# Kernel tuning notes

Hardware: AMD Instinct MI355X
Metric: run time of the kernel (lower is better)

The kernel has to match this reference:

```python
import jax, jax.numpy as jnp
import numpy as np

K = 5        # kernel_size per pseudo-dim
DIM = 2      # pseudo-coordinate dimensionality
K2 = K * K   # total kernel weight matrices
N_NODES = 50000


def spline_basis(edge_attr):
    """Open B-spline basis, degree=1, dim=2. Returns basis [E,4], weight_index [E,4]."""
    v = edge_attr * (K - 1)                      # [E,2], pseudo in [0,1]
    lo = jnp.floor(v)
    frac = v - lo                                # [E,2]
    lo = lo.astype(jnp.int32)
    fac = jnp.stack([1.0 - frac, frac], axis=-1)                 # [E,2,2] (dim, bit)
    idx = jnp.clip(lo[..., None] + jnp.arange(2), 0, K - 1)      # [E,2,2]
    b0 = jnp.array([0, 1, 0, 1])  # bit for dim 0, per spline term
    b1 = jnp.array([0, 0, 1, 1])  # bit for dim 1
    basis = fac[:, 0, b0] * fac[:, 1, b1]        # [E,4]
    wi = idx[:, 0, b0] * K + idx[:, 1, b1]       # [E,4] flat kernel index
    return basis, wi


def spline_conv(x, src, dst, basis, wi, W, root, bias, n_nodes):
    """SplineConv with mean aggregation, root weight and bias.
    x:[N,Fin] W:[K2,Fin,Fout] root:[Fin,Fout] bias:[Fout]"""
    E = src.shape[0]
    K2_, Fin, Fout = W.shape
    # scatter the 4 sparse basis values into a dense per-edge kernel-coeff matrix [E,K2]
    coeff = jnp.zeros((E, K2_), x.dtype).at[jnp.arange(E)[:, None], wi].add(basis)
    xj = x[src]                                  # gather source features [E,Fin]
    msg = jnp.zeros((E, Fout), x.dtype)
    for k in range(K2_):                         # fixed small loop over 25 kernels
        msg = msg + coeff[:, k:k + 1] * (xj @ W[k])
    agg = jax.ops.segment_sum(msg, dst, num_segments=n_nodes)    # [N,Fout]
    deg = jax.ops.segment_sum(jnp.ones((E,), x.dtype), dst, num_segments=n_nodes)
    agg = agg / jnp.clip(deg, 1.0)[:, None]      # mean aggregation
    return agg + x @ root + bias


def setup_inputs() -> dict:
    key = jax.random.key(0)
    ks = jax.random.split(key, 9)
    E = 800000
    Fin, H, C = 64, 16, 7
    x = jax.random.normal(ks[0], (N_NODES, Fin), dtype=jnp.float32)
    edge_index = jax.random.randint(ks[1], (2, E), 0, N_NODES, dtype=jnp.int64)
    edge_attr = jax.random.uniform(ks[2], (E, DIM), dtype=jnp.float32)
    s1 = 1.0 / np.sqrt(Fin)
    s2 = 1.0 / np.sqrt(H)
    W1 = jax.random.uniform(ks[3], (K2, Fin, H), jnp.float32, -s1, s1)
    root1 = jax.random.uniform(ks[4], (Fin, H), jnp.float32, -s1, s1)
    bias1 = jax.random.uniform(ks[5], (H,), jnp.float32, -s1, s1)
    W2 = jax.random.uniform(ks[6], (K2, H, C), jnp.float32, -s2, s2)
    root2 = jax.random.uniform(ks[7], (H, C), jnp.float32, -s2, s2)
    bias2 = jax.random.uniform(ks[8], (C,), jnp.float32, -s2, s2)
    return {"x": x, "edge_index": edge_index, "edge_attr": edge_attr,
            "W1": W1, "root1": root1, "bias1": bias1,
            "W2": W2, "root2": root2, "bias2": bias2}


def reference(x, edge_index, edge_attr, W1, root1, bias1, W2, root2, bias2):
    src = edge_index[0]
    dst = edge_index[1]
    basis, wi = spline_basis(edge_attr)
    h = jax.nn.relu(spline_conv(x, src, dst, basis, wi, W1, root1, bias1, N_NODES))
    # dropout(p=0.6) is identity in eval mode
    out = spline_conv(h, src, dst, basis, wi, W2, root2, bias2, N_NODES)
    return jax.nn.log_softmax(out, axis=1)
```

## Files before the change

### kernel.cpp

```cpp
#include <hip/hip_runtime.h>

#define KK2 25
#define FIN 64
#define HH 16
#define CC 7

#define SCAN_VPT 4
#define SCAN_BLK 256
#define SCAN_CHUNK (SCAN_VPT * SCAN_BLK)

__device__ inline unsigned short f2bf(float f) {
    unsigned u = __float_as_uint(f);
    return (unsigned short)((u + 0x7FFFu + ((u >> 16) & 1u)) >> 16);
}
__device__ inline float bf2f(unsigned short b) {
    return __uint_as_float(((unsigned)b) << 16);
}

__global__ void k_hist(const int* __restrict__ ei, int* __restrict__ cnt, int E) {
    int e = blockIdx.x * 256 + threadIdx.x;
    if (e < E) atomicAdd(&cnt[ei[E + e]], 1);
}

__global__ void k_bsum(const int* __restrict__ cnt, int* __restrict__ bsum, int N) {
    int b = blockIdx.x, t = threadIdx.x;
    int base = b * SCAN_CHUNK + t * SCAN_VPT;
    int s = 0;
#pragma unroll
    for (int j = 0; j < SCAN_VPT; j++) {
        int i = base + j;
        if (i < N) s += cnt[i];
    }
#pragma unroll
    for (int d = 1; d < 64; d <<= 1) s += __shfl_xor(s, d, 64);
    __shared__ int sd[SCAN_BLK / 64];
    if ((t & 63) == 0) sd[t >> 6] = s;
    __syncthreads();
    if (t == 0) {
        int tot = 0;
        for (int w = 0; w < SCAN_BLK / 64; w++) tot += sd[w];
        bsum[b] = tot;
    }
}

__global__ void k_bscan(const int* __restrict__ bsum, int* __restrict__ boff, int nblk) {
    int t = threadIdx.x;
    __shared__ int sd[256];
    int v = (t < nblk) ? bsum[t] : 0;
    sd[t] = v;
    __syncthreads();
    for (int off = 1; off < 256; off <<= 1) {
        int u = (t >= off) ? sd[t - off] : 0;
        __syncthreads();
        sd[t] += u;
        __syncthreads();
    }
    boff[t] = sd[t] - v;
}

__global__ void k_sfin(const int* __restrict__ cnt, const int* __restrict__ boff,
                       int* __restrict__ rowStart, int* __restrict__ cursor, int N) {
    int b = blockIdx.x, t = threadIdx.x;
    int base = b * SCAN_CHUNK + t * SCAN_VPT;
    int v[SCAN_VPT];
    int s = 0;
#pragma unroll
    for (int j = 0; j < SCAN_VPT; j++) {
        int i = base + j;
        v[j] = (i < N) ? cnt[i] : 0;
        s += v[j];
    }
    __shared__ int sd[SCAN_BLK];
    sd[t] = s;
    __syncthreads();
    for (int off = 1; off < SCAN_BLK; off <<= 1) {
        int u = (t >= off) ? sd[t - off] : 0;
        __syncthreads();
        sd[t] += u;
        __syncthreads();
    }
    int run = sd[t] - s + boff[b];
#pragma unroll
    for (int j = 0; j < SCAN_VPT; j++) {
        int i = base + j;
        if (i < N) {
            rowStart[i] = run;
            cursor[i] = run;
            run += v[j];
            if (i == N - 1) rowStart[N] = run;
        }
    }
}

__global__ void k_scatter(const float* __restrict__ attr, const int* __restrict__ ei,
                          int* __restrict__ cursor, uint4* __restrict__ rec, int E) {
    int e = blockIdx.x * 256 + threadIdx.x;
    if (e >= E) return;
    float v0 = attr[2 * e] * 4.0f, v1 = attr[2 * e + 1] * 4.0f;
    float l0 = floorf(v0), l1 = floorf(v1);
    float f0 = v0 - l0, f1 = v1 - l1;
    int i0 = (int)l0, i1 = (int)l1;
    int i0a = min(max(i0, 0), 4), i0b = min(max(i0 + 1, 0), 4);
    int i1a = min(max(i1, 0), 4);
    float bx = (1.0f - f0) * (1.0f - f1);
    float by = f0 * (1.0f - f1);
    float bz = (1.0f - f0) * f1;
    float bw = f0 * f1;
    unsigned pA = (unsigned)(i0a * 5 + i1a);
    unsigned pB = (unsigned)(i0b * 5 + i1a);
    int s = ei[e], d = ei[E + e];
    int pos = atomicAdd(&cursor[d], 1);
    uint4 r;
    r.x = (unsigned)f2bf(bx) | ((unsigned)f2bf(by) << 16);
    r.y = (unsigned)f2bf(bz) | ((unsigned)f2bf(bw) << 16);
    r.z = (unsigned)s;
    r.w = pA | (pB << 8);
    rec[pos] = r;
}

__global__ void k_prepW(const float* __restrict__ W1, const float* __restrict__ W2,
                        float* __restrict__ B1t, float* __restrict__ W2p) {
    int tid = blockIdx.x * 256 + threadIdx.x;
    if (tid < KK2 * FIN * HH) {
        int c = tid >> 6, i = tid & 63;
        int k = c >> 4, h = c & 15;
        B1t[tid] = W1[(k * FIN + i) * HH + h];
    }
    if (tid < KK2 * HH * 8) {
        int k = tid >> 7, r = tid & 127;
        int i = r >> 3, c = r & 7;
        W2p[tid] = (c < CC) ? W2[(k * HH + i) * CC + c] : 0.0f;
    }
}

__global__ void k_y1(const float* __restrict__ x, const float* __restrict__ B1t,
                     unsigned short* __restrict__ y1q, int N, int nbl) {
    __shared__ uint4 sh[4][2][144];
    int i0 = blockIdx.x / nbl;
    int nwin = blockIdx.x % nbl;
    int n = nwin * 256 + threadIdx.x;
    int wv = threadIdx.x >> 6, lane = threadIdx.x & 63;
    bool active = (n < N);
    float4 xr[16];
    if (active) {
        const float4* xp = (const float4*)(x + (size_t)n * 64);
#pragma unroll
        for (int i = 0; i < 16; i++) xr[i] = xp[i];
    }
    int nwb = nwin * 256 + wv * 64;
    int validf = min(64, max(0, N - nwb)) * 4;
    size_t NN = (size_t)N;

    for (int i1 = 0; i1 < 5; i1++) {
        int k = i0 * 5 + i1;
        const float* B = B1t + k * 16 * 64;
        unsigned tmp[8];
        if (active) {
#pragma unroll
            for (int h4 = 0; h4 < 4; h4++) {
                float a0 = 0, a1 = 0, a2 = 0, a3 = 0;
                const float4* b0 = (const float4*)(B + (h4 * 4 + 0) * 64);
                const float4* b1 = (const float4*)(B + (h4 * 4 + 1) * 64);
                const float4* b2 = (const float4*)(B + (h4 * 4 + 2) * 64);
                const float4* b3 = (const float4*)(B + (h4 * 4 + 3) * 64);
#pragma unroll
                for (int i = 0; i < 16; i++) {
                    float4 xi = xr[i];
                    float4 v0 = b0[i], v1 = b1[i], v2 = b2[i], v3 = b3[i];
                    a0 += xi.x * v0.x + xi.y * v0.y + xi.z * v0.z + xi.w * v0.w;
                    a1 += xi.x * v1.x + xi.y * v1.y + xi.z * v1.z + xi.w * v1.w;
                    a2 += xi.x * v2.x + xi.y * v2.y + xi.z * v2.z + xi.w * v2.w;
                    a3 += xi.x * v3.x + xi.y * v3.y + xi.z * v3.z + xi.w * v3.w;
                }
                tmp[h4 * 2 + 0] = (unsigned)f2bf(a0) | ((unsigned)f2bf(a1) << 16);
                tmp[h4 * 2 + 1] = (unsigned)f2bf(a2) | ((unsigned)f2bf(a3) << 16);
            }
        } else {
#pragma unroll
            for (int j = 0; j < 8; j++) tmp[j] = 0;
        }
        int slot = i1 & 1;
        int i0e = lane * 2, i1e = lane * 2 + 1;
        sh[wv][slot][i0e + (i0e >> 3)] = make_uint4(tmp[0], tmp[1], tmp[2], tmp[3]);
        sh[wv][slot][i1e + (i1e >> 3)] = make_uint4(tmp[4], tmp[5], tmp[6], tmp[7]);
        __syncthreads();
        if (i1 >= 1) {
            int p = i0 * 5 + (i1 - 1);
            uint4* g4 = (uint4*)(y1q + ((size_t)p * NN + nwb) * 32);
#pragma unroll
            for (int j = 0; j < 4; j++) {
                int f = j * 64 + lane;
                if (f < validf) {
                    int node = f >> 2, piece = f & 3;
                    int idx = node * 2 + (piece & 1);
                    int ss = (piece < 2) ? (slot ^ 1) : slot;
                    g4[f] = sh[wv][ss][idx + (idx >> 3)];
                }
            }
        }
        if (i1 == 4) {
            int p = i0 * 5 + 4;
            uint4* g4 = (uint4*)(y1q + ((size_t)p * NN + nwb) * 32);
#pragma unroll
            for (int j = 0; j < 4; j++) {
                int f = j * 64 + lane;
                if (f < validf) {
                    int node = f >> 2, piece = f & 3;
                    int idx = node * 2 + (piece & 1);
                    g4[f] = sh[wv][slot][idx + (idx >> 3)];
                }
            }
        }
        __syncthreads();
    }
}

__global__ void k_agg1u(const int* __restrict__ rowStart, const uint4* __restrict__ rec,
                        const unsigned short* __restrict__ y1q, const float* __restrict__ x,
                        const float* __restrict__ root1, const float* __restrict__ bias1,
                        float* __restrict__ h1, int N) {
    int n = blockIdx.x * 4 + (threadIdx.x >> 6);
    if (n >= N) return;
    int lane = threadIdx.x & 63;
    int sub = lane >> 4, h = lane & 15;
    int start = rowStart[n], end = rowStart[n + 1];
    float acc = 0.0f;
    size_t NN = (size_t)N;
    for (int i = start + sub; i < end; i += 4) {
        uint4 r = rec[i];
        float bx = bf2f((unsigned short)(r.x & 0xffffu));
        float by = bf2f((unsigned short)(r.x >> 16));
        float bz = bf2f((unsigned short)(r.y & 0xffffu));
        float bw = bf2f((unsigned short)(r.y >> 16));
        int s = (int)r.z;
        unsigned w = r.w;
        const unsigned short* rA = y1q + ((w & 255u) * NN + s) * 32;
        const unsigned short* rB = y1q + (((w >> 8) & 255u) * NN + s) * 32;
        acc += bx * bf2f(rA[h]) + bz * bf2f(rA[16 + h]);
        acc += by * bf2f(rB[h]) + bw * bf2f(rB[16 + h]);
    }
    acc += __shfl_xor(acc, 16, 64);
    acc += __shfl_xor(acc, 32, 64);
    float inv = 1.0f / (float)max(end - start, 1);
    float rv = acc * inv + bias1[h];
    const float* xrow = x + (size_t)n * 64;
#pragma unroll 8
    for (int i = 0; i < 64; i++) rv += xrow[i] * root1[i * 16 + h];
    rv = fmaxf(rv, 0.0f);
    if (lane < 16) h1[(size_t)n * 16 + h] = rv;
}

__global__ void k_y2(const float* __restrict__ h1, const float* __restrict__ W2p,
                     unsigned short* __restrict__ y2Tb, int N, int nbl) {
    int kg = blockIdx.x / nbl;
    int n = (blockIdx.x % nbl) * 256 + threadIdx.x;
    if (n >= N) return;
    float hreg[16];
    const float4* hp = (const float4*)(h1 + (size_t)n * 16);
#pragma unroll
    for (int j = 0; j < 4; j++) {
        float4 v = hp[j];
        hreg[4 * j] = v.x; hreg[4 * j + 1] = v.y;
        hreg[4 * j + 2] = v.z; hreg[4 * j + 3] = v.w;
    }
#pragma unroll
    for (int dk = 0; dk < 5; dk++) {
        int k = kg * 5 + dk;
        float z[8] = {0, 0, 0, 0, 0, 0, 0, 0};
        const float4* wp = (const float4*)(W2p + k * 128);
#pragma unroll
        for (int i = 0; i < 16; i++) {
            float hi = hreg[i];
            float4 lo = wp[2 * i], hv = wp[2 * i + 1];
            z[0] += hi * lo.x; z[1] += hi * lo.y; z[2] += hi * lo.z; z[3] += hi * lo.w;
            z[4] += hi * hv.x; z[5] += hi * hv.y; z[6] += hi * hv.z; z[7] += hi * hv.w;
        }
        uint4 p;
        p.x = (unsigned)f2bf(z[0]) | ((unsigned)f2bf(z[1]) << 16);
        p.y = (unsigned)f2bf(z[2]) | ((unsigned)f2bf(z[3]) << 16);
        p.z = (unsigned)f2bf(z[4]) | ((unsigned)f2bf(z[5]) << 16);
        p.w = (unsigned)f2bf(z[6]) | ((unsigned)f2bf(z[7]) << 16);
        *(uint4*)(y2Tb + ((size_t)k * N + n) * 8) = p;
    }
}

__global__ void k_agg2f(const int* __restrict__ rowStart, const uint4* __restrict__ rec,
                        const unsigned short* __restrict__ y2Tb, const float* __restrict__ h1,
                        const float* __restrict__ root2, const float* __restrict__ bias2,
                        float* __restrict__ out, int N) {
    int n = blockIdx.x * 4 + (threadIdx.x >> 6);
    if (n >= N) return;
    int lane = threadIdx.x & 63;
    int sub = lane >> 3, c = lane & 7;
    int start = rowStart[n], end = rowStart[n + 1];
    float acc = 0.0f;
    size_t NN = (size_t)N;
    for (int i = start + sub; i < end; i += 8) {
        uint4 r = rec[i];
        float bx = bf2f((unsigned short)(r.x & 0xffffu));
        float by = bf2f((unsigned short)(r.x >> 16));
        float bz = bf2f((unsigned short)(r.y & 0xffffu));
        float bw = bf2f((unsigned short)(r.y >> 16));
        int s = (int)r.z;
        unsigned pA = r.w & 255u, pB = (r.w >> 8) & 255u;
        unsigned i1a = pA % 5u;
        unsigned d = (i1a < 4u) ? 1u : 0u;
        acc += bx * bf2f(y2Tb[(pA * NN + s) * 8 + c]);
        acc += by * bf2f(y2Tb[(pB * NN + s) * 8 + c]);
        acc += bz * bf2f(y2Tb[((pA + d) * NN + s) * 8 + c]);
        acc += bw * bf2f(y2Tb[((pB + d) * NN + s) * 8 + c]);
    }
    acc += __shfl_xor(acc, 8, 64);
    acc += __shfl_xor(acc, 16, 64);
    acc += __shfl_xor(acc, 32, 64);
    float inv = 1.0f / (float)max(end - start, 1);
    float z;
    if (c < CC) {
        z = acc * inv + bias2[c];
        const float* hrow = h1 + (size_t)n * 16;
#pragma unroll
        for (int i = 0; i < 16; i++) z += hrow[i] * root2[i * CC + c];
    } else {
        z = -1e30f;
    }
    float m = z;
    m = fmaxf(m, __shfl_xor(m, 1, 64));
    m = fmaxf(m, __shfl_xor(m, 2, 64));
    m = fmaxf(m, __shfl_xor(m, 4, 64));
    float ex = (c < CC) ? expf(z - m) : 0.0f;
    float ssum = ex;
    ssum += __shfl_xor(ssum, 1, 64);
    ssum += __shfl_xor(ssum, 2, 64);
    ssum += __shfl_xor(ssum, 4, 64);
    float ls = logf(ssum);
    if (lane < CC) out[(size_t)n * 7 + c] = z - m - ls;
}

extern "C" void kernel_launch(void* const* d_in, const int* in_sizes, int n_in,
                              void* d_out, int out_size, void* d_ws, size_t ws_size,
                              hipStream_t stream) {
    const float* x     = (const float*)d_in[0];
    const int*   ei    = (const int*)d_in[1];
    const float* attr  = (const float*)d_in[2];
    const float* W1    = (const float*)d_in[3];
    const float* root1 = (const float*)d_in[4];
    const float* bias1 = (const float*)d_in[5];
    const float* W2    = (const float*)d_in[6];
    const float* root2 = (const float*)d_in[7];
    const float* bias2 = (const float*)d_in[8];
    float* out = (float*)d_out;

    int N = in_sizes[0] / FIN;
    int E = in_sizes[1] / 2;

    char* w = (char*)d_ws;
    size_t off = 0;
    auto alloc = [&](size_t bytes) -> void* {
        void* p = w + off;
        off += (bytes + 255) & ~(size_t)255;
        return p;
    };
    int*      cnt      = (int*)alloc((size_t)N * 4);
    int*      rowStart = (int*)alloc((size_t)(N + 1) * 4);
    int*      cursor   = (int*)alloc((size_t)N * 4);
    int*      bsum     = (int*)alloc(260 * 4);
    int*      boff     = (int*)alloc(260 * 4);
    uint4*    rec      = (uint4*)alloc((size_t)E * 16);
    float*    h1       = (float*)alloc((size_t)N * 64);
    float*    B1t      = (float*)alloc((size_t)KK2 * FIN * HH * 4);
    float*    W2p      = (float*)alloc((size_t)KK2 * HH * 8 * 4);
    unsigned short* y1q  = (unsigned short*)alloc((size_t)KK2 * N * 32 * 2);
    unsigned short* y2Tb = y1q;
    (void)ws_size; (void)n_in; (void)out_size;

    hipMemsetAsync(cnt, 0, (size_t)N * 4, stream);

    int ebl = (E + 255) / 256;
    int nbl = (N + 255) / 256;
    int sblk = (N + SCAN_CHUNK - 1) / SCAN_CHUNK;

    k_hist<<<ebl, 256, 0, stream>>>(ei, cnt, E);
    k_bsum<<<sblk, SCAN_BLK, 0, stream>>>(cnt, bsum, N);
    k_bscan<<<1, 256, 0, stream>>>(bsum, boff, sblk);
    k_sfin<<<sblk, SCAN_BLK, 0, stream>>>(cnt, boff, rowStart, cursor, N);
    k_scatter<<<ebl, 256, 0, stream>>>(attr, ei, cursor, rec, E);
    k_prepW<<<(KK2 * FIN * HH + 255) / 256, 256, 0, stream>>>(W1, W2, B1t, W2p);
    k_y1<<<5 * nbl, 256, 0, stream>>>(x, B1t, y1q, N, nbl);
    k_agg1u<<<(N + 3) / 4, 256, 0, stream>>>(rowStart, rec, y1q, x, root1, bias1, h1, N);
    k_y2<<<5 * nbl, 256, 0, stream>>>(h1, W2p, y2Tb, N, nbl);
    k_agg2f<<<(N + 3) / 4, 256, 0, stream>>>(rowStart, rec, y2Tb, h1, root2, bias2, out, N);
}
```

Before: 289.2 us.

## Store layer-1 per-kernel projections node-major and unroll edge gather loop

Changes the y1 intermediate from kernel-major [K2][N][32] to node-major [N][800] bf16, so all 25 kernel projections of a source node sit contiguously. The layer-1 gather then reads both kernel rows for an edge from the same 1.6 KB node block, which should improve cache and DRAM locality. The aggregation loop is also unrolled by two edges per lane-group with separate accumulators to raise memory-level parallelism. The k_y1 writes become strided by 100 uint4 per node, so that write pass loses its coalescing. y2Tb still aliases the buffer and k_y2 is unchanged.

```diff
diff --git a/kernel.cpp b/kernel.cpp
--- a/kernel.cpp
+++ b/kernel.cpp
@@ -134,7 +134,7 @@
 }
 
 __global__ void k_y1(const float* __restrict__ x, const float* __restrict__ B1t,
-                     unsigned short* __restrict__ y1q, int N, int nbl) {
+                     unsigned short* __restrict__ y1n, int N, int nbl) {
     __shared__ uint4 sh[4][2][144];
     int i0 = blockIdx.x / nbl;
     int nwin = blockIdx.x % nbl;
@@ -149,7 +149,6 @@
     }
     int nwb = nwin * 256 + wv * 64;
     int validf = min(64, max(0, N - nwb)) * 4;
-    size_t NN = (size_t)N;
 
     for (int i1 = 0; i1 < 5; i1++) {
         int k = i0 * 5 + i1;
@@ -186,28 +185,28 @@
         __syncthreads();
         if (i1 >= 1) {
             int p = i0 * 5 + (i1 - 1);
-            uint4* g4 = (uint4*)(y1q + ((size_t)p * NN + nwb) * 32);
+            uint4* g4 = (uint4*)y1n;
 #pragma unroll
             for (int j = 0; j < 4; j++) {
                 int f = j * 64 + lane;
                 if (f < validf) {
-                    int node = f >> 2, piece = f & 3;
-                    int idx = node * 2 + (piece & 1);
-                    int ss = (piece < 2) ? (slot ^ 1) : slot;
-                    g4[f] = sh[wv][ss][idx + (idx >> 3)];
+                    int m = f >> 2, q = f & 3;
+                    int idx = m * 2 + (q & 1);
+                    int ss = (q < 2) ? (slot ^ 1) : slot;
+                    g4[(size_t)(nwb + m) * 100 + p * 4 + q] = sh[wv][ss][idx + (idx >> 3)];
                 }
             }
         }
         if (i1 == 4) {
             int p = i0 * 5 + 4;
-            uint4* g4 = (uint4*)(y1q + ((size_t)p * NN + nwb) * 32);
+            uint4* g4 = (uint4*)y1n;
 #pragma unroll
             for (int j = 0; j < 4; j++) {
                 int f = j * 64 + lane;
                 if (f < validf) {
-                    int node = f >> 2, piece = f & 3;
-                    int idx = node * 2 + (piece & 1);
-                    g4[f] = sh[wv][slot][idx + (idx >> 3)];
+                    int m = f >> 2, q = f & 3;
+                    int idx = m * 2 + (q & 1);
+                    g4[(size_t)(nwb + m) * 100 + p * 4 + q] = sh[wv][slot][idx + (idx >> 3)];
                 }
             }
         }
@@ -216,7 +215,7 @@
 }
 
 __global__ void k_agg1u(const int* __restrict__ rowStart, const uint4* __restrict__ rec,
-                        const unsigned short* __restrict__ y1q, const float* __restrict__ x,
+                        const unsigned short* __restrict__ y1n, const float* __restrict__ x,
                         const float* __restrict__ root1, const float* __restrict__ bias1,
                         float* __restrict__ h1, int N) {
     int n = blockIdx.x * 4 + (threadIdx.x >> 6);
@@ -224,28 +223,51 @@
     int lane = threadIdx.x & 63;
     int sub = lane >> 4, h = lane & 15;
     int start = rowStart[n], end = rowStart[n + 1];
-    float acc = 0.0f;
-    size_t NN = (size_t)N;
-    for (int i = start + sub; i < end; i += 4) {
+    float acc0 = 0.0f, acc1 = 0.0f;
+    int i = start + sub;
+    for (; i + 4 < end; i += 8) {
+        uint4 r0 = rec[i];
+        uint4 r1 = rec[i + 4];
+        {
+            int s = (int)r0.z;
+            unsigned w = r0.w;
+            const unsigned short* rA = y1n + (size_t)s * 800 + (w & 255u) * 32;
+            const unsigned short* rB = y1n + (size_t)s * 800 + ((w >> 8) & 255u) * 32;
+            acc0 += bf2f((unsigned short)(r0.x & 0xffffu)) * bf2f(rA[h])
+                  + bf2f((unsigned short)(r0.y & 0xffffu)) * bf2f(rA[16 + h])
+                  + bf2f((unsigned short)(r0.x >> 16)) * bf2f(rB[h])
+                  + bf2f((unsigned short)(r0.y >> 16)) * bf2f(rB[16 + h]);
+        }
+        {
+            int s = (int)r1.z;
+            unsigned w = r1.w;
+            const unsigned short* rA = y1n + (size_t)s * 800 + (w & 255u) * 32;
+            const unsigned short* rB = y1n + (size_t)s * 800 + ((w >> 8) & 255u) * 32;
+            acc1 += bf2f((unsigned short)(r1.x & 0xffffu)) * bf2f(rA[h])
+                  + bf2f((unsigned short)(r1.y & 0xffffu)) * bf2f(rA[16 + h])
+                  + bf2f((unsigned short)(r1.x >> 16)) * bf2f(rB[h])
+                  + bf2f((unsigned short)(r1.y >> 16)) * bf2f(rB[16 + h]);
+        }
+    }
+    for (; i < end; i += 4) {
         uint4 r = rec[i];
-        float bx = bf2f((unsigned short)(r.x & 0xffffu));
-        float by = bf2f((unsigned short)(r.x >> 16));
-        float bz = bf2f((unsigned short)(r.y & 0xffffu));
-        float bw = bf2f((unsigned short)(r.y >> 16));
         int s = (int)r.z;
         unsigned w = r.w;
-        const unsigned short* rA = y1q + ((w & 255u) * NN + s) * 32;
-        const unsigned short* rB = y1q + (((w >> 8) & 255u) * NN + s) * 32;
-        acc += bx * bf2f(rA[h]) + bz * bf2f(rA[16 + h]);
-        acc += by * bf2f(rB[h]) + bw * bf2f(rB[16 + h]);
-    }
+        const unsigned short* rA = y1n + (size_t)s * 800 + (w & 255u) * 32;
+        const unsigned short* rB = y1n + (size_t)s * 800 + ((w >> 8) & 255u) * 32;
+        acc0 += bf2f((unsigned short)(r.x & 0xffffu)) * bf2f(rA[h])
+              + bf2f((unsigned short)(r.y & 0xffffu)) * bf2f(rA[16 + h])
+              + bf2f((unsigned short)(r.x >> 16)) * bf2f(rB[h])
+              + bf2f((unsigned short)(r.y >> 16)) * bf2f(rB[16 + h]);
+    }
+    float acc = acc0 + acc1;
     acc += __shfl_xor(acc, 16, 64);
     acc += __shfl_xor(acc, 32, 64);
     float inv = 1.0f / (float)max(end - start, 1);
     float rv = acc * inv + bias1[h];
     const float* xrow = x + (size_t)n * 64;
 #pragma unroll 8
-    for (int i = 0; i < 64; i++) rv += xrow[i] * root1[i * 16 + h];
+    for (int ii = 0; ii < 64; ii++) rv += xrow[ii] * root1[ii * 16 + h];
     rv = fmaxf(rv, 0.0f);
     if (lane < 16) h1[(size_t)n * 16 + h] = rv;
 }
@@ -369,8 +391,8 @@
     float*    h1       = (float*)alloc((size_t)N * 64);
     float*    B1t      = (float*)alloc((size_t)KK2 * FIN * HH * 4);
     float*    W2p      = (float*)alloc((size_t)KK2 * HH * 8 * 4);
-    unsigned short* y1q  = (unsigned short*)alloc((size_t)KK2 * N * 32 * 2);
-    unsigned short* y2Tb = y1q;
+    unsigned short* y1n  = (unsigned short*)alloc((size_t)N * 800 * 2);
+    unsigned short* y2Tb = y1n;
     (void)ws_size; (void)n_in; (void)out_size;
 
     hipMemsetAsync(cnt, 0, (size_t)N * 4, stream);
@@ -385,8 +407,8 @@
     k_sfin<<<sblk, SCAN_BLK, 0, stream>>>(cnt, boff, rowStart, cursor, N);
     k_scatter<<<ebl, 256, 0, stream>>>(attr, ei, cursor, rec, E);
     k_prepW<<<(KK2 * FIN * HH + 255) / 256, 256, 0, stream>>>(W1, W2, B1t, W2p);
-    k_y1<<<5 * nbl, 256, 0, stream>>>(x, B1t, y1q, N, nbl);
-    k_agg1u<<<(N + 3) / 4, 256, 0, stream>>>(rowStart, rec, y1q, x, root1, bias1, h1, N);
+    k_y1<<<5 * nbl, 256, 0, stream>>>(x, B1t, y1n, N, nbl);
+    k_agg1u<<<(N + 3) / 4, 256, 0, stream>>>(rowStart, rec, y1n, x, root1, bias1, h1, N);
     k_y2<<<5 * nbl, 256, 0, stream>>>(h1, W2p, y2Tb, N, nbl);
     k_agg2f<<<(N + 3) / 4, 256, 0, stream>>>(rowStart, rec, y2Tb, h1, root2, bias2, out, N);
 }
```

Result: no change. 287.0 us (median of 2 runs) (-0.8%).
